# Kernel optimization log

Hardware: AMD Instinct MI355X
Metric: run time of the kernel (lower is better)

## Reference

```python
import jax, jax.numpy as jnp
import numpy as np

V = 8000      # output_size (vocab)
EMB = 256     # emb_size
ENC = 512     # enc_hid_size
DEC = 512     # dec_hid_size
HE = 20       # energizer hidden (fixed in source)


def setup_inputs() -> dict:
    key = jax.random.key(0)
    ks = jax.random.split(key, 12)
    B, S, T = 64, 128, 128
    s = 0.05
    return {
        "enc_hid": jax.random.normal(ks[0], (B, S, ENC), dtype=jnp.float32),
        "real_output": jax.random.randint(ks[1], (B, T), 0, V),
        "W_e1": jax.random.normal(ks[2], (ENC + DEC, HE), dtype=jnp.float32) * s,
        "b_e1": jnp.zeros((HE,), jnp.float32),
        "W_e2": jax.random.normal(ks[3], (HE, 1), dtype=jnp.float32) * s,
        "b_e2": jnp.zeros((1,), jnp.float32),
        "emb": jax.random.normal(ks[4], (V, EMB), dtype=jnp.float32) * s,
        "W_rnn": jax.random.normal(ks[5], (EMB + DEC + ENC, DEC), dtype=jnp.float32) * s,
        "b_rnn": jnp.zeros((DEC,), jnp.float32),
        "W_out": jax.random.normal(ks[6], (EMB + DEC + ENC, V), dtype=jnp.float32) * s,
        "b_out": jnp.zeros((V,), jnp.float32),
    }


def _decode(enc_hid, real_output, W_e1, b_e1, W_e2, b_e2, emb, W_rnn, b_rnn, W_out, b_out):
    B, S, _ = enc_hid.shape

    def step(carry, y_i):
        last_char, last_hidden = carry  # [B] int, [B,DEC]
        # additive attention, vectorized over all encoder positions
        hid_b = jnp.broadcast_to(last_hidden[:, None, :], (B, S, DEC))
        cat = jnp.concatenate([enc_hid, hid_b], axis=-1)          # [B,S,ENC+DEC]
        e = jax.nn.elu(cat @ W_e1 + b_e1)                          # [B,S,HE]
        e = jax.nn.elu(e @ W_e2 + b_e2)[..., 0]                    # [B,S]
        ew = jnp.exp(e)
        w = ew / jnp.sum(ew, axis=1, keepdims=True)                # [B,S]
        context = jnp.einsum('bs,bse->be', w, enc_hid)             # [B,ENC]
        last_ch = emb[last_char % V]                               # [B,EMB]
        new_hidden = jax.nn.elu(
            jnp.concatenate([last_ch, last_hidden, context], axis=1) @ W_rnn + b_rnn)
        out = jax.nn.elu(
            jnp.concatenate([last_ch, new_hidden, context], axis=1) @ W_out + b_out)
        # teacher_forcing_prob = 1.0 -> next char is the ground truth token
        return (y_i, new_hidden), (out, w)

    init = (jnp.zeros((B,), real_output.dtype), jnp.zeros((B, DEC), enc_hid.dtype))
    _, (outs, weights) = jax.lax.scan(step, init, real_output.T)   # [T,B,V], [T,B,S]
    return outs.transpose(1, 0, 2), weights.transpose(1, 0, 2)


def reference(enc_hid, real_output, W_e1, b_e1, W_e2, b_e2, emb, W_rnn, b_rnn, W_out, b_out):
    return _decode(enc_hid, real_output, W_e1, b_e1, W_e2, b_e2, emb,
                   W_rnn, b_rnn, W_out, b_out)
```

## Files before the change

### kernel.cpp

```cpp
#include <hip/hip_runtime.h>
#include <hip/hip_bf16.h>
#include <stdint.h>

#define BATCH 64
#define SLEN 128
#define TLEN 128
#define ENCD 512
#define DECD 512
#define EMBD 256
#define VOC  8000
#define HE   20
#define KX   1280
#define NPAD 8064

typedef __attribute__((ext_vector_type(8))) short short8;
typedef __attribute__((ext_vector_type(8))) _Float16 half8v;
typedef __attribute__((ext_vector_type(4))) float f32x4;
typedef _Float16 h2 __attribute__((ext_vector_type(2)));

__device__ inline unsigned short f2bf(float f) {
  union { float f; uint32_t u; } v; v.f = f;
  uint32_t r = v.u + 0x7fff + ((v.u >> 16) & 1);
  return (unsigned short)(r >> 16);
}
__device__ inline unsigned short f16bits(float f) {
  union { _Float16 h; unsigned short u; } c; c.h = (_Float16)f; return c.u;
}
__device__ inline uint32_t pkh2(float a, float b) {
  union { h2 h; uint32_t u; } v;
  v.h = h2{(_Float16)a, (_Float16)b};
  return v.u;
}
__device__ inline float fdot2(uint32_t a, uint32_t b, float c) {
#if __has_builtin(__builtin_amdgcn_fdot2)
  union { uint32_t u; h2 h; } x, y; x.u = a; y.u = b;
  return __builtin_amdgcn_fdot2(x.h, y.h, c, false);
#else
  union { uint32_t u; h2 h; } x, y; x.u = a; y.u = b;
  return c + (float)x.h[0] * (float)y.h[0] + (float)x.h[1] * (float)y.h[1];
#endif
}
__device__ inline float eluf(float x) { return x > 0.f ? x : (expf(x) - 1.f); }

typedef const __attribute__((address_space(1))) unsigned int* gptr_t;
typedef __attribute__((address_space(3))) unsigned int* lptr_t;
__device__ inline void gload16(const void* g, void* l) {
  __builtin_amdgcn_global_load_lds((gptr_t)g, (lptr_t)l, 16, 0, 0);
}

__global__ __launch_bounds__(256) void k_e1(const float* __restrict__ enc,
                                            const float* __restrict__ We1,
                                            float* __restrict__ E1) {
  __shared__ float rowbuf[4][ENCD];
  __shared__ float part[4][HE][2];
  int r0 = blockIdx.x * 4;
  int tid = threadIdx.x;
  for (int i = tid; i < 4 * ENCD; i += 256) {
    int rl = i >> 9, e = i & 511;
    rowbuf[rl][e] = enc[(size_t)(r0 + rl) * ENCD + e];
  }
  __syncthreads();
  if (tid < 160) {
    int kg = tid / 80, rem = tid % 80, rl = rem / 20, h = rem % 20;
    float acc = 0.f;
    for (int k = kg * 256; k < kg * 256 + 256; ++k)
      acc += rowbuf[rl][k] * We1[k * HE + h];
    part[rl][h][kg] = acc;
  }
  __syncthreads();
  if (tid < 80) {
    int rl = tid / 20, h = tid % 20;
    int r = r0 + rl, bb = r >> 7, ss = r & 127;
    E1[((size_t)bb * HE + h) * SLEN + ss] = part[rl][h][0] + part[rl][h][1];
  }
}

__global__ __launch_bounds__(256) void k_tr_wout(const float* __restrict__ Wo,
                                                 unsigned short* __restrict__ WoT) {
  __shared__ float tile[64][65];
  int n0 = blockIdx.x * 64, k0 = blockIdx.y * 64;
  int tid = threadIdx.x;
  for (int i = tid; i < 4096; i += 256) {
    int kk = i >> 6, nn = i & 63;
    int n = n0 + nn;
    tile[kk][nn] = (n < VOC) ? Wo[(size_t)(k0 + kk) * VOC + n] : 0.f;
  }
  __syncthreads();
  for (int i = tid; i < 4096; i += 256) {
    int nn = i >> 6, kk = i & 63;
    WoT[(size_t)(n0 + nn) * KX + k0 + kk] = f2bf(tile[kk][nn]);
  }
}

__global__ __launch_bounds__(256) void k_tr_w(const float* __restrict__ src,
                                              unsigned short* __restrict__ dst,
                                              int k0, int KN, int fmt) {
  __shared__ float tile[64][65];
  int n0 = blockIdx.x * 64, kt = blockIdx.y * 64;
  int tid = threadIdx.x;
  for (int i = tid; i < 4096; i += 256) {
    int kk = i >> 6, nn = i & 63;
    tile[kk][nn] = src[(size_t)(k0 + kt + kk) * 512 + n0 + nn];
  }
  __syncthreads();
  for (int i = tid; i < 4096; i += 256) {
    int nn = i >> 6, kk = i & 63;
    float v = tile[kk][nn];
    dst[(size_t)(n0 + nn) * KN + kt + kk] = fmt ? f2bf(v) : f16bits(v);
  }
}

__global__ __launch_bounds__(256) void k_prep_wr(const float* __restrict__ Wr,
                                                 unsigned short* __restrict__ W2) {
  int i = blockIdx.x * 256 + threadIdx.x;
  int n = i & 511;
  int j = (i >> 9) & 7;
  int kc = (i >> 12) & 31;
  int h = (i >> 17) & 1;
  int k = h * 256 + kc * 8 + j;
  W2[(((size_t)(h * 32 + kc) * 512) + n) * 8 + j] = f16bits(Wr[(size_t)(256 + k) * 512 + n]);
}

__global__ __launch_bounds__(256) void k_ench(const float* __restrict__ enc,
                                              unsigned short* __restrict__ ench) {
  int i = (blockIdx.x * 256 + threadIdx.x) * 4;
  float4 v = *(const float4*)(enc + i);
  ushort4 o = { f16bits(v.x), f16bits(v.y), f16bits(v.z), f16bits(v.w) };
  *(ushort4*)(ench + i) = o;
}

__global__ __launch_bounds__(256) void k_wh(const float* __restrict__ wout,
                                            unsigned short* __restrict__ wh) {
  int i = (blockIdx.x * 256 + threadIdx.x) * 4;
  float4 v = *(const float4*)(wout + i);
  ushort4 o = { f16bits(v.x), f16bits(v.y), f16bits(v.z), f16bits(v.w) };
  *(ushort4*)(wh + i) = o;
}

__global__ __launch_bounds__(256) void k_tr_encb(const float* __restrict__ enc,
                                                 unsigned short* __restrict__ encT) {
  __shared__ float tile[64][65];
  int b = blockIdx.x, e0 = blockIdx.y * 64, s0 = blockIdx.z * 64;
  int tid = threadIdx.x;
  const float* eb = enc + (size_t)b * SLEN * ENCD;
  for (int i = tid; i < 4096; i += 256) {
    int ss = i >> 6, ee = i & 63;
    tile[ss][ee] = eb[(size_t)(s0 + ss) * ENCD + e0 + ee];
  }
  __syncthreads();
  unsigned short* ob = encT + (size_t)b * ENCD * SLEN;
  for (int i = tid; i < 4096; i += 256) {
    int ee = i >> 6, ss = i & 63;
    ob[(size_t)(e0 + ee) * SLEN + s0 + ss] = f16bits(tile[ss][ee]);
  }
}

__global__ __launch_bounds__(256) void k_lc(const int* __restrict__ ro,
                                            const float* __restrict__ emb,
                                            unsigned short* __restrict__ X) {
  int r = blockIdx.x;
  int t = r >> 6, b = r & 63;
  int lc = (t == 0) ? 0 : ro[b * TLEN + t - 1];
  lc = ((lc % VOC) + VOC) % VOC;
  X[(size_t)r * KX + threadIdx.x] = f2bf(emb[(size_t)lc * EMBD + threadIdx.x]);
}

#define BM 128
#define BN 128
#define BK 64

template<int MODE>
__global__ __launch_bounds__(256) void k_gs(
    const unsigned short* __restrict__ A,
    const unsigned short* __restrict__ B,
    const float* __restrict__ bias,
    unsigned short* __restrict__ Cout)
{
  constexpr int As = (MODE == 0) ? KX : (MODE == 1 ? 512 : 128);
  constexpr int Bs = (MODE == 0) ? 256 : (MODE == 1 ? 512 : 128);
  constexpr int KT = (MODE == 0) ? 4 : (MODE == 1 ? 8 : 2);
  __shared__ __align__(16) unsigned short Asd[BM * BK];
  __shared__ __align__(16) unsigned short Bsd[BN * BK];
  int bx = blockIdx.x, by = blockIdx.y;
  int tid = threadIdx.x;
  int wid = tid >> 6, lane = tid & 63;
  int wr = wid >> 1, wc = wid & 1;

  f32x4 acc[4][4];
  for (int i = 0; i < 4; ++i)
    for (int j = 0; j < 4; ++j) acc[i][j] = (f32x4)0.f;

  const unsigned short* Abase = A + (size_t)by * BM * As;
  const unsigned short* Bbase = B + (size_t)bx * BN * Bs + (MODE == 2 ? (size_t)by * 512 * 128 : 0);

  for (int kt = 0; kt < KT; ++kt) {
    for (int j = 0; j < 4; ++j) {
      int c = tid + j * 256;
      int r = c >> 3, c16 = c & 7;
      int sk = c16 ^ (r & 7);
      gload16(Abase + (size_t)r * As + kt * BK + sk * 8, (char*)Asd + c * 16);
      gload16(Bbase + (size_t)r * Bs + kt * BK + sk * 8, (char*)Bsd + c * 16);
    }
    __syncthreads();
    for (int ks = 0; ks < 2; ++ks) {
      short8 af[4], bf[4];
      int kc = ks * 4 + (lane >> 4);
      for (int i = 0; i < 4; ++i) {
        int r = wr * 64 + i * 16 + (lane & 15);
        af[i] = *(const short8*)((const char*)Asd + r * 128 + ((kc ^ (r & 7)) * 16));
      }
      for (int j = 0; j < 4; ++j) {
        int r = wc * 64 + j * 16 + (lane & 15);
        bf[j] = *(const short8*)((const char*)Bsd + r * 128 + ((kc ^ (r & 7)) * 16));
      }
      for (int i = 0; i < 4; ++i)
        for (int j = 0; j < 4; ++j) {
          if constexpr (MODE == 0)
            acc[i][j] = __builtin_amdgcn_mfma_f32_16x16x32_bf16(af[i], bf[j], acc[i][j], 0, 0, 0);
          else
            acc[i][j] = __builtin_amdgcn_mfma_f32_16x16x32_f16(
                __builtin_bit_cast(half8v, af[i]), __builtin_bit_cast(half8v, bf[j]), acc[i][j], 0, 0, 0);
        }
    }
    __syncthreads();
  }

  int rl = lane >> 4, cl = lane & 15;
  for (int j = 0; j < 4; ++j) {
    int gn = bx * BN + wc * 64 + j * 16 + cl;
    for (int i = 0; i < 4; ++i) {
      for (int q = 0; q < 4; ++q) {
        int gm = by * BM + wr * 64 + i * 16 + rl * 4 + q;
        float v = acc[i][j][q];
        if constexpr (MODE == 0) {
          Cout[(size_t)gm * 512 + gn] = f16bits(v + bias[gn]);
        } else if constexpr (MODE == 1) {
          int bb = gm >> 7, s = gm & 127;
          Cout[(((size_t)(bb * 16 + (s >> 3)) * 512) + gn) * 8 + (s & 7)] = f16bits(v);
        } else {
          int tt = gm & 127, bb = gm >> 7;
          Cout[((size_t)tt * 64 + bb) * KX + 768 + gn] = f2bf(v);
        }
      }
    }
  }
}

__global__ __launch_bounds__(1024) void k_recur(
    const float* __restrict__ We1,
    const float* __restrict__ be1,
    const float* __restrict__ We2,
    const float* __restrict__ be2,
    const uint4* __restrict__ W2,
    const uint4* __restrict__ encW2,
    const unsigned short* __restrict__ Remb,
    const float* __restrict__ E1g,
    unsigned short* __restrict__ X,
    float* __restrict__ wout)
{
  __shared__ __align__(16) uint4 el[16][512];
  __shared__ uint32_t E1p[HE][SLEN / 2];
  __shared__ uint32_t w1p[HE][257];
  __shared__ uint32_t hpair[DECD / 2];
  __shared__ uint32_t wpairS[SLEN / 2];
  __shared__ float ph[2][DECD];
  __shared__ float be1s[HE], w2s[HE];
  __shared__ float be2s;

  int b = blockIdx.x, tid = threadIdx.x;

  for (int i = tid; i < 16 * 512; i += 1024) ((uint4*)el)[i] = encW2[(size_t)b * 8192 + i];
  for (int i = tid; i < HE * (SLEN / 2); i += 1024) {
    int h = i >> 6, p = i & 63;
    const float* ebase = E1g + ((size_t)b * HE + h) * SLEN;
    ((uint32_t*)E1p)[i] = pkh2(ebase[2 * p], ebase[2 * p + 1]);
  }
  for (int i = tid; i < HE * 256; i += 1024) {
    int h = i >> 8, p = i & 255;
    w1p[h][p] = pkh2(We1[(size_t)(ENCD + 2 * p) * HE + h],
                     We1[(size_t)(ENCD + 2 * p + 1) * HE + h]);
  }
  for (int i = tid; i < DECD / 2; i += 1024) hpair[i] = 0;
  for (int i = tid; i < DECD; i += 1024) { ph[0][i] = 0.f; ph[1][i] = 0.f; }
  if (tid < HE) { be1s[tid] = be1[tid]; w2s[tid] = We2[tid]; }
  if (tid == 0) be2s = be2[0];
  __syncthreads();

  const int lane = tid & 63;
  const bool attn_wave = (tid >= 960);
  int mn, mh0, mblocks;
  if (tid < 448)      { mn = tid;              mh0 = 0; mblocks = 4; }
  else if (tid < 896) { mn = tid - 448;        mh0 = 1; mblocks = 4; }
  else if (tid < 960) { mn = 448 + (tid - 896); mh0 = 0; mblocks = 8; }
  else                { mn = 0;                mh0 = 0; mblocks = 0; }
  const uint4* Wp = W2 + (size_t)(mh0 * 32) * 512 + mn;
  const uint4* hp4 = (const uint4*)hpair;
  const int hbase = mh0 * 32;

  int ah = lane % 20, aseg = lane / 20;
  int q0 = aseg * 86;
  int q1 = (aseg == 2) ? 256 : q0 + 86;
  if (aseg >= 3) { q0 = 0; q1 = 0; }

  for (int t = 0; t < TLEN; ++t) {
    const int rowr = t * BATCH + b;
    float rpre = 0.f;

    if (!attn_wave) {
      if (tid < 512) {
        union { unsigned short u; _Float16 f; } c;
        c.u = Remb[(size_t)rowr * 512 + tid];
        rpre = (float)c.f;
      }
      float a0 = 0, a1 = 0, a2 = 0, a3 = 0;
      uint4 cb[8], nb[8];
      #pragma unroll
      for (int j = 0; j < 8; ++j) cb[j] = Wp[(size_t)j * 512];
      for (int blk = 0; blk < mblocks; ++blk) {
        if (blk + 1 < mblocks) {
          #pragma unroll
          for (int j = 0; j < 8; ++j) nb[j] = Wp[(size_t)((blk + 1) * 8 + j) * 512];
        }
        #pragma unroll
        for (int j = 0; j < 8; ++j) {
          uint4 wv = cb[j]; uint4 xv = hp4[hbase + blk * 8 + j];
          a0 = fdot2(wv.x, xv.x, a0); a1 = fdot2(wv.y, xv.y, a1);
          a2 = fdot2(wv.z, xv.z, a2); a3 = fdot2(wv.w, xv.w, a3);
        }
        #pragma unroll
        for (int j = 0; j < 8; ++j) cb[j] = nb[j];
      }
      ph[mh0][mn] = (a0 + a1) + (a2 + a3);
    } else {
      __builtin_amdgcn_s_setprio(1);
      float p0 = 0, p1 = 0;
      for (int q = q0; q < q1; q += 2) {
        p0 = fdot2(w1p[ah][q], hpair[q], p0);
        p1 = fdot2(w1p[ah][q + 1], hpair[q + 1], p1);
      }
      float p = p0 + p1;
      float pa = __shfl(p, lane + 20);
      float pb = __shfl(p, lane + 40);
      float edv = p + pa + pb + ((lane < HE) ? be1s[lane] : 0.f);
      float e0a = 0.f, e1a = 0.f;
      #pragma unroll
      for (int h = 0; h < HE; ++h) {
        union { uint32_t u; h2 hh; } e; e.u = E1p[h][lane];
        float ed = __shfl(edv, h);
        e0a += eluf((float)e.hh[0] + ed) * w2s[h];
        e1a += eluf((float)e.hh[1] + ed) * w2s[h];
      }
      float s0 = expf(eluf(e0a + be2s));
      float s1 = expf(eluf(e1a + be2s));
      float tot = s0 + s1;
      #pragma unroll
      for (int o = 1; o < 64; o <<= 1) tot += __shfl_xor(tot, o);
      float inv = 1.f / tot;
      float w0 = s0 * inv, w1 = s1 * inv;
      wpairS[lane] = pkh2(w0, w1);
      float2 wv2 = { w0, w1 };
      *(float2*)(wout + ((size_t)b * TLEN + t) * SLEN + 2 * lane) = wv2;
      __builtin_amdgcn_s_setprio(0);
    }
    __syncthreads();

    if (tid < 512) {
      int n = tid;
      float c0 = 0, c1 = 0, c2 = 0, c3 = 0;
      #pragma unroll
      for (int g = 0; g < 16; ++g) {
        uint4 ev = el[g][n];
        uint4 wv = ((const uint4*)wpairS)[g];
        c0 = fdot2(ev.x, wv.x, c0); c1 = fdot2(ev.y, wv.y, c1);
        c2 = fdot2(ev.z, wv.z, c2); c3 = fdot2(ev.w, wv.w, c3);
      }
      float v = rpre + ph[0][n] + ph[1][n] + (c0 + c1) + (c2 + c3);
      float aa = eluf(v);
      X[(size_t)rowr * KX + 256 + n] = f2bf(aa);
      float bb = __shfl_down(aa, 1);
      if (!(n & 1)) hpair[n >> 1] = pkh2(aa, bb);
    }
    __syncthreads();
  }
}

__global__ __launch_bounds__(256) void k_gemm(
    const unsigned short* __restrict__ Xb,
    const unsigned short* __restrict__ WoT,
    const float* __restrict__ bout,
    float* __restrict__ out)
{
  __shared__ __align__(16) unsigned short As[BM * BK];
  __shared__ __align__(16) unsigned short Bs[BN * BK];
  int bid = blockIdx.x;
  int swz = (bid & 7) * 504 + (bid >> 3);
  int bx = swz % 63;
  int by = swz / 63;
  int tid = threadIdx.x;
  int wid = tid >> 6, lane = tid & 63;
  int wr = wid >> 1, wc = wid & 1;

  f32x4 acc[4][4];
  for (int i = 0; i < 4; ++i)
    for (int j = 0; j < 4; ++j) acc[i][j] = (f32x4)0.f;

  const unsigned short* Abase = Xb + (size_t)by * BM * KX;
  const unsigned short* Bbase = WoT + (size_t)bx * BN * KX;

  for (int kt = 0; kt < KX / BK; ++kt) {
    for (int j = 0; j < 4; ++j) {
      int c = tid + j * 256;
      int r = c >> 3, c16 = c & 7;
      int sk = c16 ^ (r & 7);
      gload16(Abase + (size_t)r * KX + kt * BK + sk * 8, (char*)As + c * 16);
      gload16(Bbase + (size_t)r * KX + kt * BK + sk * 8, (char*)Bs + c * 16);
    }
    __syncthreads();
    for (int ks = 0; ks < 2; ++ks) {
      short8 af[4], bf[4];
      int kc = ks * 4 + (lane >> 4);
      for (int i = 0; i < 4; ++i) {
        int r = wr * 64 + i * 16 + (lane & 15);
        af[i] = *(const short8*)((const char*)As + r * 128 + ((kc ^ (r & 7)) * 16));
      }
      for (int j = 0; j < 4; ++j) {
        int r = wc * 64 + j * 16 + (lane & 15);
        bf[j] = *(const short8*)((const char*)Bs + r * 128 + ((kc ^ (r & 7)) * 16));
      }
      for (int i = 0; i < 4; ++i)
        for (int j = 0; j < 4; ++j)
          acc[i][j] = __builtin_amdgcn_mfma_f32_16x16x32_bf16(af[i], bf[j], acc[i][j], 0, 0, 0);
    }
    __syncthreads();
  }

  int rl = lane >> 4, cl = lane & 15;
  for (int j = 0; j < 4; ++j) {
    int gn = bx * BN + wc * 64 + j * 16 + cl;
    if (gn >= VOC) continue;
    float bv = bout[gn];
    for (int i = 0; i < 4; ++i) {
      for (int q = 0; q < 4; ++q) {
        int gm = by * BM + wr * 64 + i * 16 + rl * 4 + q;
        int tt = gm >> 6, bb = gm & 63;
        float v = acc[i][j][q] + bv;
        v = v > 0.f ? v : (expf(v) - 1.f);
        out[((size_t)bb * TLEN + tt) * VOC + gn] = v;
      }
    }
  }
}

extern "C" void kernel_launch(void* const* d_in, const int* in_sizes, int n_in,
                              void* d_out, int out_size, void* d_ws, size_t ws_size,
                              hipStream_t stream) {
  const float* enc  = (const float*)d_in[0];
  const int*   ro   = (const int*)d_in[1];
  const float* We1  = (const float*)d_in[2];
  const float* be1  = (const float*)d_in[3];
  const float* We2  = (const float*)d_in[4];
  const float* be2  = (const float*)d_in[5];
  const float* emb  = (const float*)d_in[6];
  const float* Wr   = (const float*)d_in[7];
  const float* brnn = (const float*)d_in[8];
  const float* Wo   = (const float*)d_in[9];
  const float* bo   = (const float*)d_in[10];

  char* ws = (char*)d_ws;
  unsigned short* X     = (unsigned short*)(ws);
  unsigned short* WoT   = (unsigned short*)(ws + 20971520);
  unsigned short* W2    = (unsigned short*)(ws + 41615360);
  unsigned short* WembT = (unsigned short*)(ws + 42139648);
  unsigned short* WctxT = (unsigned short*)(ws + 42401792);
  unsigned short* ench  = (unsigned short*)(ws + 42926080);
  float*          E1    = (float*)(ws + 51314688);
  unsigned short* Remb  = (unsigned short*)(ws + 51970048);
  unsigned short* encW2 = (unsigned short*)(ws + 60358656);
  unsigned short* encTh = ench;
  unsigned short* wh    = Remb;

  float* outs = (float*)d_out;
  float* wout = (float*)d_out + (size_t)BATCH * TLEN * VOC;

  k_lc     <<<dim3(8192),     256, 0, stream>>>(ro, emb, X);
  k_e1     <<<dim3(2048),     256, 0, stream>>>(enc, We1, E1);
  k_tr_wout<<<dim3(126, 20),  256, 0, stream>>>(Wo, WoT);
  k_tr_w   <<<dim3(8, 4),     256, 0, stream>>>(Wr, WembT, 0, 256, 1);
  k_tr_w   <<<dim3(8, 8),     256, 0, stream>>>(Wr, WctxT, 768, 512, 0);
  k_prep_wr<<<dim3(1024),     256, 0, stream>>>(Wr, W2);
  k_ench   <<<dim3(4096),     256, 0, stream>>>(enc, ench);
  k_gs<0>  <<<dim3(4, 64),    256, 0, stream>>>(X, WembT, brnn, Remb);
  k_gs<1>  <<<dim3(4, 64),    256, 0, stream>>>(ench, WctxT, brnn, encW2);
  k_recur  <<<dim3(64),      1024, 0, stream>>>(We1, be1, We2, be2,
                                                (const uint4*)W2, (const uint4*)encW2,
                                                Remb, E1, X, wout);
  k_wh     <<<dim3(1024),     256, 0, stream>>>(wout, wh);
  k_tr_encb<<<dim3(64, 8, 2), 256, 0, stream>>>(enc, encTh);
  k_gs<2>  <<<dim3(4, 64),    256, 0, stream>>>(wh, encTh, brnn, X);
  k_gemm   <<<dim3(4032),     256, 0, stream>>>(X, WoT, bo, outs);
  (void)in_sizes; (void)n_in; (void)out_size; (void)ws_size;
}
```

Baseline: 1.398 ms.

## Stream recurrent weights and encoder context through per-wave async LDS rings

The recurrent kernel drops its register double-buffered global loads of the hidden-to-hidden weights. Instead each wave streams them into its own 8-slot LDS ring with direct global-to-LDS loads and explicit vmcnt waits. The encoder context block is no longer kept resident in LDS. Its loads are issued before the barrier and consumed from the same ring afterwards, and the embedding-preactivation load moves after the barrier. The aim is to hide per-step global latency and cut register pressure, at the cost of re-reading encoder data every step and relying on fragile hand-counted waitcnt ordering.

```diff
diff --git a/kernel.cpp b/kernel.cpp
--- a/kernel.cpp
+++ b/kernel.cpp
@@ -246,6 +246,24 @@
   }
 }
 
+#define WAITV(n) asm volatile("s_waitcnt vmcnt(" #n ")" ::: "memory")
+#define ISSA(J) gload16((const char*)W2 + (((size_t)(hbase + (J)) * 512 + mn) * 16), \
+                        (char*)ring + wv_ * 8192 + ((J) & 7) * 1024)
+#define CONSA(J, WN, R) { WAITV(WN); \
+  uint4 tv = ring[wv_][(J) & 7][lane]; uint4 xv = hp4[hbase + (J)]; \
+  a0 = fdot2(tv.x, xv.x, a0); a1 = fdot2(tv.y, xv.y, a1); \
+  a2 = fdot2(tv.z, xv.z, a2); a3 = fdot2(tv.w, xv.w, a3); \
+  if ((J) + 8 < (R)) ISSA((J) + 8); }
+#define CA8(J, R) CONSA(J,7,R) CONSA((J)+1,7,R) CONSA((J)+2,7,R) CONSA((J)+3,7,R) \
+                  CONSA((J)+4,7,R) CONSA((J)+5,7,R) CONSA((J)+6,7,R) CONSA((J)+7,7,R)
+#define ISSB(J) gload16((const char*)encW2b + (((size_t)(J) * 512 + tid) * 16), \
+                        (char*)ring + wv_ * 8192 + ((J) & 7) * 1024)
+#define CONSB(J, WN) { WAITV(WN); \
+  uint4 ev = ring[wv_][(J) & 7][lane]; uint4 wq = ((const uint4*)wpairS)[J]; \
+  c0 = fdot2(ev.x, wq.x, c0); c1 = fdot2(ev.y, wq.y, c1); \
+  c2 = fdot2(ev.z, wq.z, c2); c3 = fdot2(ev.w, wq.w, c3); \
+  if ((J) + 8 < 16) ISSB((J) + 8); }
+
 __global__ __launch_bounds__(1024) void k_recur(
     const float* __restrict__ We1,
     const float* __restrict__ be1,
@@ -258,7 +276,7 @@
     unsigned short* __restrict__ X,
     float* __restrict__ wout)
 {
-  __shared__ __align__(16) uint4 el[16][512];
+  __shared__ __align__(16) uint4 ring[16][8][64];
   __shared__ uint32_t E1p[HE][SLEN / 2];
   __shared__ uint32_t w1p[HE][257];
   __shared__ uint32_t hpair[DECD / 2];
@@ -268,8 +286,8 @@
   __shared__ float be2s;
 
   int b = blockIdx.x, tid = threadIdx.x;
-
-  for (int i = tid; i < 16 * 512; i += 1024) ((uint4*)el)[i] = encW2[(size_t)b * 8192 + i];
+  const uint4* encW2b = encW2 + (size_t)b * 8192;
+
   for (int i = tid; i < HE * (SLEN / 2); i += 1024) {
     int h = i >> 6, p = i & 63;
     const float* ebase = E1g + ((size_t)b * HE + h) * SLEN;
@@ -287,13 +305,11 @@
   __syncthreads();
 
   const int lane = tid & 63;
-  const bool attn_wave = (tid >= 960);
-  int mn, mh0, mblocks;
-  if (tid < 448)      { mn = tid;              mh0 = 0; mblocks = 4; }
-  else if (tid < 896) { mn = tid - 448;        mh0 = 1; mblocks = 4; }
-  else if (tid < 960) { mn = 448 + (tid - 896); mh0 = 0; mblocks = 8; }
-  else                { mn = 0;                mh0 = 0; mblocks = 0; }
-  const uint4* Wp = W2 + (size_t)(mh0 * 32) * 512 + mn;
+  const int wv_ = tid >> 6;
+  int mn, mh0;
+  if (tid < 448)      { mn = tid;               mh0 = 0; }
+  else if (tid < 896) { mn = tid - 448;         mh0 = 1; }
+  else                { mn = 448 + lane;        mh0 = 0; }
   const uint4* hp4 = (const uint4*)hpair;
   const int hbase = mh0 * 32;
 
@@ -304,34 +320,8 @@
 
   for (int t = 0; t < TLEN; ++t) {
     const int rowr = t * BATCH + b;
-    float rpre = 0.f;
-
-    if (!attn_wave) {
-      if (tid < 512) {
-        union { unsigned short u; _Float16 f; } c;
-        c.u = Remb[(size_t)rowr * 512 + tid];
-        rpre = (float)c.f;
-      }
-      float a0 = 0, a1 = 0, a2 = 0, a3 = 0;
-      uint4 cb[8], nb[8];
-      #pragma unroll
-      for (int j = 0; j < 8; ++j) cb[j] = Wp[(size_t)j * 512];
-      for (int blk = 0; blk < mblocks; ++blk) {
-        if (blk + 1 < mblocks) {
-          #pragma unroll
-          for (int j = 0; j < 8; ++j) nb[j] = Wp[(size_t)((blk + 1) * 8 + j) * 512];
-        }
-        #pragma unroll
-        for (int j = 0; j < 8; ++j) {
-          uint4 wv = cb[j]; uint4 xv = hp4[hbase + blk * 8 + j];
-          a0 = fdot2(wv.x, xv.x, a0); a1 = fdot2(wv.y, xv.y, a1);
-          a2 = fdot2(wv.z, xv.z, a2); a3 = fdot2(wv.w, xv.w, a3);
-        }
-        #pragma unroll
-        for (int j = 0; j < 8; ++j) cb[j] = nb[j];
-      }
-      ph[mh0][mn] = (a0 + a1) + (a2 + a3);
-    } else {
+
+    if (wv_ == 15) {
       __builtin_amdgcn_s_setprio(1);
       float p0 = 0, p1 = 0;
       for (int q = q0; q < q1; q += 2) {
@@ -361,19 +351,40 @@
       float2 wv2 = { w0, w1 };
       *(float2*)(wout + ((size_t)b * TLEN + t) * SLEN + 2 * lane) = wv2;
       __builtin_amdgcn_s_setprio(0);
+    } else if (wv_ == 14) {
+      float a0 = 0, a1 = 0, a2 = 0, a3 = 0;
+      ISSA(0); ISSA(1); ISSA(2); ISSA(3); ISSA(4); ISSA(5); ISSA(6); ISSA(7);
+      CA8(0, 64) CA8(8, 64) CA8(16, 64) CA8(24, 64)
+      CA8(32, 64) CA8(40, 64) CA8(48, 64)
+      CONSA(56, 7, 64) CONSA(57, 6, 64) CONSA(58, 5, 64) CONSA(59, 4, 64)
+      CONSA(60, 3, 64) CONSA(61, 2, 64) CONSA(62, 1, 64) CONSA(63, 0, 64)
+      ph[0][mn] = (a0 + a1) + (a2 + a3);
+    } else {
+      float a0 = 0, a1 = 0, a2 = 0, a3 = 0;
+      ISSA(0); ISSA(1); ISSA(2); ISSA(3); ISSA(4); ISSA(5); ISSA(6); ISSA(7);
+      CA8(0, 32) CA8(8, 32) CA8(16, 32)
+      CONSA(24, 7, 32) CONSA(25, 6, 32) CONSA(26, 5, 32) CONSA(27, 4, 32)
+      CONSA(28, 3, 32) CONSA(29, 2, 32) CONSA(30, 1, 32) CONSA(31, 0, 32)
+      ph[mh0][mn] = (a0 + a1) + (a2 + a3);
+      if (wv_ < 8) {
+        ISSB(0); ISSB(1); ISSB(2); ISSB(3); ISSB(4); ISSB(5); ISSB(6); ISSB(7);
+      }
     }
     __syncthreads();
 
     if (tid < 512) {
+      float rpre;
+      {
+        union { unsigned short u; _Float16 f; } c;
+        c.u = Remb[(size_t)rowr * 512 + tid];
+        rpre = (float)c.f;
+      }
+      float c0 = 0, c1 = 0, c2 = 0, c3 = 0;
+      CONSB(0, 7) CONSB(1, 7) CONSB(2, 7) CONSB(3, 7) CONSB(4, 7)
+      CONSB(5, 7) CONSB(6, 7) CONSB(7, 7) CONSB(8, 7)
+      CONSB(9, 6) CONSB(10, 5) CONSB(11, 4) CONSB(12, 3)
+      CONSB(13, 2) CONSB(14, 1) CONSB(15, 0)
       int n = tid;
-      float c0 = 0, c1 = 0, c2 = 0, c3 = 0;
-      #pragma unroll
-      for (int g = 0; g < 16; ++g) {
-        uint4 ev = el[g][n];
-        uint4 wv = ((const uint4*)wpairS)[g];
-        c0 = fdot2(ev.x, wv.x, c0); c1 = fdot2(ev.y, wv.y, c1);
-        c2 = fdot2(ev.z, wv.z, c2); c3 = fdot2(ev.w, wv.w, c3);
-      }
       float v = rpre + ph[0][n] + ph[1][n] + (c0 + c1) + (c2 + c3);
       float aa = eluf(v);
       X[(size_t)rowr * KX + 256 + n] = f2bf(aa);
```

Measured after the change: 2.645 ms. 1.89x slower.
